# Kernel optimization log

Measured on AMD Instinct MI355X. Metric: run time of the kernel, lower is better.

Reference implementation:

```python
import jax, jax.numpy as jnp
import numpy as np

B, S, HID = 1, 4096, 2048
NH, NKV, D = 16, 4, 128           # num_heads, num_kv_heads, head_dim
QPG = NH // NKV                   # q heads per kv group
GROUP = (QPG + 2) * D             # fused per-group width: Q..Q K V
TOTAL = NKV * GROUP


def setup_inputs() -> dict:
    key = jax.random.key(0)
    k0, k1, k2 = jax.random.split(key, 3)
    x = jax.random.normal(k0, (B, S, HID), dtype=jnp.float32)
    weight_qkv = jax.random.normal(k1, (TOTAL, HID), dtype=jnp.float32) * 0.02
    weight_proj = jax.random.normal(k2, (HID, NH * D), dtype=jnp.float32) * 0.02
    return {"x": x, "weight_qkv": weight_qkv, "weight_proj": weight_proj}


def reference(x, weight_qkv, weight_proj):
    b, s, _ = x.shape
    # fused QKV projection, grouped layout: [b, s, NKV, (QPG+2)*D]
    qkv = jnp.einsum('bsh,ph->bsp', x, weight_qkv).reshape(b, s, NKV, GROUP)
    q = qkv[..., : QPG * D].reshape(b, s, NKV, QPG, D)      # [b,s,g,q,d]
    k = qkv[..., QPG * D:(QPG + 1) * D]                      # [b,s,g,d]
    v = qkv[..., (QPG + 1) * D:]                             # [b,s,g,d]

    scale = 1.0 / jnp.sqrt(jnp.float32(D))
    # GQA causal attention (ring attention at cp_size=1 == full causal attn)
    scores = jnp.einsum('bsgqd,btgd->bgqst', q, k) * scale   # [b,g,q,s,s]
    causal = jnp.tril(jnp.ones((s, s), dtype=bool))
    scores = jnp.where(causal, scores, jnp.finfo(scores.dtype).min)
    attn = jax.nn.softmax(scores, axis=-1)
    out = jnp.einsum('bgqst,btgd->bsgqd', attn, v)           # [b,s,g,q,d]
    out = out.reshape(b, s, NH * D)
    return jnp.einsum('bse,he->bsh', out, weight_proj)       # [b,s,HID]
```

## Files before the change

kernel.cpp:

```cpp
#include <hip/hip_runtime.h>
#include <hip/hip_bf16.h>
#include <stdint.h>

typedef __attribute__((ext_vector_type(8))) short short8;
typedef __attribute__((ext_vector_type(4))) float f32x4;

#define S_LEN   4096
#define HID_DIM 2048
#define NHEAD   16
#define NKV     4
#define DHEAD   128
#define QPG     4
#define GROUP   768
#define TOTAL   3072

#define NSLOT   336

__device__ __forceinline__ ushort f2bf(float f) {
    union { float f; uint32_t u; } c; c.f = f;
    uint32_t u = c.u;
    u += 0x7fff + ((u >> 16) & 1);
    return (ushort)(u >> 16);
}

__device__ __forceinline__ void gld_lds16(const void* g, void* l) {
    __builtin_amdgcn_global_load_lds(
        (const __attribute__((address_space(1))) void*)g,
        (__attribute__((address_space(3))) void*)l, 16, 0, 0);
}

__global__ __launch_bounds__(256)
void cvt_f32_bf16(const float* __restrict__ src, ushort* __restrict__ dst,
                  int n4, int mode)
{
    int i = blockIdx.x * blockDim.x + threadIdx.x;
    int stride = gridDim.x * blockDim.x;
    for (; i < n4; i += stride) {
        float sc = 1.0f;
        if (mode == 1) {
            int row = i >> 9;
            sc = ((row % GROUP) < QPG * DHEAD) ? 0.088388347648318447f : 1.0f;
        }
        float4 v = ((const float4*)src)[i];
        ushort4 o;
        o.x = f2bf(v.x * sc); o.y = f2bf(v.y * sc);
        o.z = f2bf(v.z * sc); o.w = f2bf(v.w * sc);
        ((ushort4*)dst)[i] = o;
    }
}

__global__ __launch_bounds__(256)
void zero_f4(float4* __restrict__ p, int n4)
{
    int i = blockIdx.x * blockDim.x + threadIdx.x;
    int stride = gridDim.x * blockDim.x;
    float4 z = {0.f, 0.f, 0.f, 0.f};
    for (; i < n4; i += stride) p[i] = z;
}

__device__ __forceinline__ void store_c(ushort* C, size_t idx, float v) { C[idx] = f2bf(v); }
__device__ __forceinline__ void store_c(float*  C, size_t idx, float v) { C[idx] = v; }

template <typename OutT, bool WRITE_VT>
__global__ __launch_bounds__(256, 2)
void gemm_bt(const ushort* __restrict__ A, const ushort* __restrict__ B,
             OutT* __restrict__ C, ushort* __restrict__ VT,
             int M, int N, int K)
{
    __shared__ alignas(16) ushort Asl[128 * 32];
    __shared__ alignas(16) ushort Bsl[128 * 32];

    const int tid  = threadIdx.x;
    const int wave = tid >> 6;
    const int lane = tid & 63;
    const int quad = lane >> 4;
    const int l15  = lane & 15;
    const int wr   = wave >> 1;
    const int wc   = wave & 1;
    const int m0   = blockIdx.y * 128;
    const int n0   = blockIdx.x * 128;

    f32x4 acc[4][4];
#pragma unroll
    for (int i = 0; i < 4; i++)
#pragma unroll
        for (int j = 0; j < 4; j++) acc[i][j] = (f32x4)0.0f;

    for (int kb = 0; kb < K; kb += 32) {
        __syncthreads();
#pragma unroll
        for (int r = 0; r < 2; r++) {
            int idx = tid + r * 256;
            int row = idx >> 2, c8 = idx & 3;
            char* la = (char*)Asl + (size_t)(wave * 64 + r * 256) * 16;
            char* lb = (char*)Bsl + (size_t)(wave * 64 + r * 256) * 16;
            gld_lds16(A + (size_t)(m0 + row) * K + kb + c8 * 8, la);
            gld_lds16(B + (size_t)(n0 + row) * K + kb + c8 * 8, lb);
        }
        __syncthreads();

        short8 af[4], bf[4];
#pragma unroll
        for (int i = 0; i < 4; i++)
            af[i] = *(const short8*)(&Asl[(wr * 64 + i * 16 + l15) * 32 + quad * 8]);
#pragma unroll
        for (int j = 0; j < 4; j++)
            bf[j] = *(const short8*)(&Bsl[(wc * 64 + j * 16 + l15) * 32 + quad * 8]);
#pragma unroll
        for (int i = 0; i < 4; i++)
#pragma unroll
            for (int j = 0; j < 4; j++)
                acc[i][j] = __builtin_amdgcn_mfma_f32_16x16x32_bf16(
                    af[i], bf[j], acc[i][j], 0, 0, 0);
    }

#pragma unroll
    for (int i = 0; i < 4; i++)
#pragma unroll
        for (int j = 0; j < 4; j++)
#pragma unroll
            for (int r = 0; r < 4; r++) {
                int row = m0 + wr * 64 + i * 16 + quad * 4 + r;
                int col = n0 + wc * 64 + j * 16 + l15;
                store_c(C, (size_t)row * N + col, acc[i][j][r]);
            }

    if (WRITE_VT) {
        int cb = n0 >> 7;
        if (cb % 6 == 5) {
            int g = cb / 6;
#pragma unroll
            for (int i = 0; i < 4; i++)
#pragma unroll
                for (int j = 0; j < 4; j++) {
                    int d    = wc * 64 + j * 16 + l15;
                    int row0 = m0 + wr * 64 + i * 16 + quad * 4;
                    ushort4 pk;
                    pk.x = f2bf(acc[i][j][0]); pk.y = f2bf(acc[i][j][1]);
                    pk.z = f2bf(acc[i][j][2]); pk.w = f2bf(acc[i][j][3]);
                    *(ushort4*)(VT + (size_t)(g * 128 + d) * S_LEN + row0) = pk;
                }
        }
    }
}

__global__ __launch_bounds__(256, 2)
void flash_attn(const ushort* __restrict__ qkv, const ushort* __restrict__ VT,
                ushort* __restrict__ out, float* __restrict__ o_slot,
                float* __restrict__ l_slot)
{
    const int b     = blockIdx.x;
    const int head  = b / 48;
    const int r48   = b - head * 48;
    const int pair  = r48 / 3;
    const int third = r48 - pair * 3;

    const int g    = head >> 2;
    const int qh   = head & 3;
    const int H    = 128 - 4 * pair;
    const int L    = 4 * pair + 4;
    const int c0   = third * 44;
    const int c1   = c0 + 44;

    const int tid  = threadIdx.x;
    const int wave = tid >> 6;
    const int lane = tid & 63;
    const int quad = lane >> 4;
    const int l15  = lane & 15;

    __shared__ alignas(16) ushort Kl[2][32][128];
    __shared__ alignas(16) ushort Vt[2][128][32];
    __shared__ alignas(16) ushort Pl[4][32][36];

    int seg_p[2], seg_t0[2], seg_t1[2], seg_slot[2];
    int nseg = 0;
    {
        int h1 = (c1 < H) ? c1 : H;
        if (c0 < h1) {
            seg_p[nseg] = 31 - pair; seg_t0[nseg] = c0; seg_t1[nseg] = h1;
            seg_slot[nseg] = head * 16 + pair;
            nseg++;
        }
        int l0 = (c0 > H) ? c0 : H;
        if (l0 < c1) {
            int lt0 = l0 - H, lt1 = c1 - H;
            int whole = (lt0 == 0) & (lt1 == L);
            seg_p[nseg] = pair; seg_t0[nseg] = lt0; seg_t1[nseg] = lt1;
            seg_slot[nseg] = whole ? -1 : (256 + head * 5 + (pair - 11));
            nseg++;
        }
    }

    const int koff = g * GROUP + QPG * DHEAD;

    for (int s = 0; s < nseg; s++) {
        const int t0 = seg_t0[s];
        const int t1 = seg_t1[s];
        const int q0 = seg_p[s] * 128;

        short8 qf[2][4];
#pragma unroll
        for (int mi = 0; mi < 2; mi++) {
            int row = q0 + wave * 32 + mi * 16 + l15;
            const ushort* qp = qkv + (size_t)row * TOTAL + g * GROUP + qh * DHEAD + quad * 8;
#pragma unroll
            for (int ks = 0; ks < 4; ks++)
                qf[mi][ks] = *(const short8*)(qp + ks * 32);
        }

        f32x4 o[2][8];
#pragma unroll
        for (int mi = 0; mi < 2; mi++)
#pragma unroll
            for (int df = 0; df < 8; df++) o[mi][df] = (f32x4)0.0f;
        float l_vec[2][4];
#pragma unroll
        for (int mi = 0; mi < 2; mi++)
#pragma unroll
            for (int r = 0; r < 4; r++) l_vec[mi][r] = 0.0f;

        const int kr = tid >> 4, kc = tid & 15;
        const int vd = tid >> 2, vc = tid & 3;

        float4 kpre[2], vpre[2];
#pragma unroll
        for (int r = 0; r < 2; r++) {
            kpre[r] = *(const float4*)(qkv + (size_t)(t0 * 32 + kr + r * 16) * TOTAL + koff + kc * 8);
            vpre[r] = *(const float4*)(VT + (size_t)(g * 128 + vd + r * 64) * S_LEN + t0 * 32 + vc * 8);
        }
#pragma unroll
        for (int r = 0; r < 2; r++) {
            int krow = kr + r * 16, vrow = vd + r * 64;
            *(float4*)(&Kl[0][krow][(kc ^ (krow & 7)) * 8]) = kpre[r];
            *(float4*)(&Vt[0][vrow][(vc ^ (vrow & 3)) * 8]) = vpre[r];
        }
        if (t0 + 1 < t1) {
            const int j1 = (t0 + 1) * 32;
#pragma unroll
            for (int r = 0; r < 2; r++) {
                kpre[r] = *(const float4*)(qkv + (size_t)(j1 + kr + r * 16) * TOTAL + koff + kc * 8);
                vpre[r] = *(const float4*)(VT + (size_t)(g * 128 + vd + r * 64) * S_LEN + j1 + vc * 8);
            }
        }
        __syncthreads();

        for (int t = t0; t < t1; t++) {
            const int cur = (t - t0) & 1;

            if (t + 1 < t1) {
#pragma unroll
                for (int r = 0; r < 2; r++) {
                    int krow = kr + r * 16, vrow = vd + r * 64;
                    *(float4*)(&Kl[cur ^ 1][krow][(kc ^ (krow & 7)) * 8]) = kpre[r];
                    *(float4*)(&Vt[cur ^ 1][vrow][(vc ^ (vrow & 3)) * 8]) = vpre[r];
                }
                if (t + 2 < t1) {
                    const int j2 = (t + 2) * 32;
#pragma unroll
                    for (int r = 0; r < 2; r++) {
                        kpre[r] = *(const float4*)(qkv + (size_t)(j2 + kr + r * 16) * TOTAL + koff + kc * 8);
                        vpre[r] = *(const float4*)(VT + (size_t)(g * 128 + vd + r * 64) * S_LEN + j2 + vc * 8);
                    }
                }
            }

            const int j0 = t * 32;
            f32x4 sacc[2][2];
#pragma unroll
            for (int mi = 0; mi < 2; mi++)
#pragma unroll
                for (int ni = 0; ni < 2; ni++) sacc[mi][ni] = (f32x4)0.0f;
            __builtin_amdgcn_s_setprio(1);
#pragma unroll
            for (int ni = 0; ni < 2; ni++)
#pragma unroll
                for (int ks = 0; ks < 4; ks++) {
                    int krow = ni * 16 + l15;
                    short8 kf = *(const short8*)(&Kl[cur][krow][((ks * 4 + quad) ^ (krow & 7)) * 8]);
#pragma unroll
                    for (int mi = 0; mi < 2; mi++)
                        sacc[mi][ni] = __builtin_amdgcn_mfma_f32_16x16x32_bf16(
                            qf[mi][ks], kf, sacc[mi][ni], 0, 0, 0);
                }
            __builtin_amdgcn_s_setprio(0);

#pragma unroll
            for (int mi = 0; mi < 2; mi++) {
                const int base = q0 + wave * 32 + mi * 16;
                if (j0 + 31 > base) {
#pragma unroll
                    for (int r = 0; r < 4; r++) {
                        int row_g = base + quad * 4 + r;
                        float rs = 0.0f;
#pragma unroll
                        for (int ni = 0; ni < 2; ni++) {
                            float e = __expf(sacc[mi][ni][r]);
                            int col_g = j0 + ni * 16 + l15;
                            e = (col_g > row_g) ? 0.0f : e;
                            sacc[mi][ni][r] = e;
                            rs += e;
                        }
                        l_vec[mi][r] += rs;
                    }
                } else {
#pragma unroll
                    for (int r = 0; r < 4; r++) {
                        float rs = 0.0f;
#pragma unroll
                        for (int ni = 0; ni < 2; ni++) {
                            float e = __expf(sacc[mi][ni][r]);
                            sacc[mi][ni][r] = e;
                            rs += e;
                        }
                        l_vec[mi][r] += rs;
                    }
                }
#pragma unroll
                for (int ni = 0; ni < 2; ni++)
#pragma unroll
                    for (int r = 0; r < 4; r++)
                        Pl[wave][mi * 16 + quad * 4 + r][ni * 16 + l15] =
                            f2bf(sacc[mi][ni][r]);
            }

            short8 pf[2];
#pragma unroll
            for (int mi = 0; mi < 2; mi++)
                pf[mi] = *(const short8*)(&Pl[wave][mi * 16 + l15][quad * 8]);
            __builtin_amdgcn_s_setprio(1);
#pragma unroll
            for (int df = 0; df < 8; df++) {
                int vrow = df * 16 + l15;
                short8 vf = *(const short8*)(&Vt[cur][vrow][(quad ^ (vrow & 3)) * 8]);
#pragma unroll
                for (int mi = 0; mi < 2; mi++)
                    o[mi][df] = __builtin_amdgcn_mfma_f32_16x16x32_bf16(
                        pf[mi], vf, o[mi][df], 0, 0, 0);
            }
            __builtin_amdgcn_s_setprio(0);

            __syncthreads();
        }

        if (seg_slot[s] >= 0) {
            const int sslot = seg_slot[s];
#pragma unroll
            for (int mi = 0; mi < 2; mi++)
#pragma unroll
                for (int r = 0; r < 4; r++) {
                    int row_l = wave * 32 + mi * 16 + quad * 4 + r;
                    float l = l_vec[mi][r];
                    l += __shfl_xor(l, 1);
                    l += __shfl_xor(l, 2);
                    l += __shfl_xor(l, 4);
                    l += __shfl_xor(l, 8);
                    if (l15 == 0)
                        atomicAdd(&l_slot[sslot * 128 + row_l], l);
#pragma unroll
                    for (int df = 0; df < 8; df++)
                        atomicAdd(&o_slot[((size_t)sslot * 128 + row_l) * 128
                                          + df * 16 + l15], o[mi][df][r]);
                }
        } else {
#pragma unroll
            for (int mi = 0; mi < 2; mi++)
#pragma unroll
                for (int r = 0; r < 4; r++) {
                    float l = l_vec[mi][r];
                    l += __shfl_xor(l, 1);
                    l += __shfl_xor(l, 2);
                    l += __shfl_xor(l, 4);
                    l += __shfl_xor(l, 8);
                    float inv = 1.0f / l;
                    int row = q0 + wave * 32 + mi * 16 + quad * 4 + r;
#pragma unroll
                    for (int df = 0; df < 8; df++) {
                        float v = o[mi][df][r] * inv;
                        out[(size_t)row * (NHEAD * DHEAD) + head * DHEAD
                            + df * 16 + l15] = f2bf(v);
                    }
                }
        }
    }
}

__global__ __launch_bounds__(256)
void fixup_norm(const float* __restrict__ o_slot, const float* __restrict__ l_slot,
                ushort* __restrict__ attn)
{
    const int slot = blockIdx.x;
    int head, q0;
    if (slot < 256) {
        head = slot >> 4;
        q0   = (31 - (slot & 15)) * 128;
    } else {
        int s = slot - 256;
        head = s / 5;
        q0   = (11 + (s - head * 5)) * 128;
    }
    const int t = threadIdx.x;
#pragma unroll 4
    for (int i = 0; i < 64; i++) {
        int idx = i * 256 + t;
        int row = idx >> 7, d = idx & 127;
        float l = l_slot[slot * 128 + row];
        float v = o_slot[(size_t)slot * 16384 + idx] / l;
        attn[(size_t)(q0 + row) * HID_DIM + head * DHEAD + d] = f2bf(v);
    }
}

extern "C" void kernel_launch(void* const* d_in, const int* in_sizes, int n_in,
                              void* d_out, int out_size, void* d_ws, size_t ws_size,
                              hipStream_t stream)
{
    const float* x     = (const float*)d_in[0];
    const float* wqkv  = (const float*)d_in[1];
    const float* wproj = (const float*)d_in[2];
    float* outp = (float*)d_out;

    const size_t n_x     = (size_t)S_LEN * HID_DIM;
    const size_t n_wqkv  = (size_t)TOTAL * HID_DIM;
    const size_t n_wproj = (size_t)HID_DIM * HID_DIM;
    const size_t n_qkv   = (size_t)S_LEN * TOTAL;
    const size_t n_attn  = (size_t)S_LEN * HID_DIM;

    ushort* xb     = (ushort*)d_ws;
    ushort* wqkvb  = xb + n_x;
    ushort* qkv    = wqkvb + n_wqkv;
    ushort* attn   = qkv + n_qkv;
    ushort* vt     = attn + n_attn;
    float* o_slot  = (float*)d_ws;
    float* l_slot  = o_slot + (size_t)NSLOT * 16384;
    ushort* wprojb = wqkvb;

    cvt_f32_bf16<<<2048, 256, 0, stream>>>(x, xb, (int)(n_x / 4), 0);
    cvt_f32_bf16<<<2048, 256, 0, stream>>>(wqkv, wqkvb, (int)(n_wqkv / 4), 1);

    gemm_bt<ushort, true><<<dim3(TOTAL / 128, S_LEN / 128), 256, 0, stream>>>(
        xb, wqkvb, qkv, vt, S_LEN, TOTAL, HID_DIM);

    zero_f4<<<2048, 256, 0, stream>>>((float4*)o_slot,
                                      (int)(((size_t)NSLOT * 16384 + NSLOT * 128) / 4));

    flash_attn<<<768, 256, 0, stream>>>(qkv, vt, attn, o_slot, l_slot);
    fixup_norm<<<NSLOT, 256, 0, stream>>>(o_slot, l_slot, attn);

    cvt_f32_bf16<<<2048, 256, 0, stream>>>(wproj, wprojb, (int)(n_wproj / 4), 0);
    gemm_bt<float, false><<<dim3(HID_DIM / 128, S_LEN / 128), 256, 0, stream>>>(
        attn, wprojb, outp, nullptr, S_LEN, HID_DIM, HID_DIM);
}
```

Before: 456.6 us.

## Compute transposed S^T tiles so P stays in registers, drop P LDS round-trip

The QK^T MFMA now has its operands swapped, so each lane holds a column of scores along the KV dimension. The exponentiated probabilities can then be packed straight into bf16 registers with v_cvt_pk_bf16 and fed to 16x16x16 MFMAs against V, with no round trip through the per-wave P scratch in LDS. The K and V tiles switch from XOR swizzling to padded rows. The end-of-iteration __syncthreads becomes an lgkmcnt wait plus s_barrier, and the output stores become 4-wide packed writes. The cost is twice as many smaller MFMAs for PV, and padded LDS rows that may leave some bank conflicts.

Measured after the change: 528.1 us. +15.7%, slower.

```diff
diff --git a/kernel.cpp b/kernel.cpp
--- a/kernel.cpp
+++ b/kernel.cpp
@@ -3,6 +3,7 @@
 #include <stdint.h>
 
 typedef __attribute__((ext_vector_type(8))) short short8;
+typedef __attribute__((ext_vector_type(4))) short bf16x4;
 typedef __attribute__((ext_vector_type(4))) float f32x4;
 
 #define S_LEN   4096
@@ -23,10 +24,20 @@
     return (ushort)(u >> 16);
 }
 
+__device__ __forceinline__ uint32_t cvt_pk_bf16(float lo, float hi) {
+    uint32_t r;
+    asm("v_cvt_pk_bf16_f32 %0, %1, %2" : "=v"(r) : "v"(lo), "v"(hi));
+    return r;
+}
+
 __device__ __forceinline__ void gld_lds16(const void* g, void* l) {
     __builtin_amdgcn_global_load_lds(
         (const __attribute__((address_space(1))) void*)g,
         (__attribute__((address_space(3))) void*)l, 16, 0, 0);
+}
+
+__device__ __forceinline__ void lds_barrier() {
+    asm volatile("s_waitcnt lgkmcnt(0)\n\ts_barrier" ::: "memory");
 }
 
 __global__ __launch_bounds__(256)
@@ -168,9 +179,8 @@
     const int quad = lane >> 4;
     const int l15  = lane & 15;
 
-    __shared__ alignas(16) ushort Kl[2][32][128];
-    __shared__ alignas(16) ushort Vt[2][128][32];
-    __shared__ alignas(16) ushort Pl[4][32][36];
+    __shared__ alignas(16) ushort Kl[2][32][136];
+    __shared__ alignas(16) ushort Vt[2][128][40];
 
     int seg_p[2], seg_t0[2], seg_t1[2], seg_slot[2];
     int nseg = 0;
@@ -200,24 +210,20 @@
 
         short8 qf[2][4];
 #pragma unroll
-        for (int mi = 0; mi < 2; mi++) {
-            int row = q0 + wave * 32 + mi * 16 + l15;
+        for (int qi = 0; qi < 2; qi++) {
+            int row = q0 + wave * 32 + qi * 16 + l15;
             const ushort* qp = qkv + (size_t)row * TOTAL + g * GROUP + qh * DHEAD + quad * 8;
 #pragma unroll
             for (int ks = 0; ks < 4; ks++)
-                qf[mi][ks] = *(const short8*)(qp + ks * 32);
+                qf[qi][ks] = *(const short8*)(qp + ks * 32);
         }
 
         f32x4 o[2][8];
 #pragma unroll
-        for (int mi = 0; mi < 2; mi++)
-#pragma unroll
-            for (int df = 0; df < 8; df++) o[mi][df] = (f32x4)0.0f;
-        float l_vec[2][4];
-#pragma unroll
-        for (int mi = 0; mi < 2; mi++)
-#pragma unroll
-            for (int r = 0; r < 4; r++) l_vec[mi][r] = 0.0f;
+        for (int qi = 0; qi < 2; qi++)
+#pragma unroll
+            for (int df = 0; df < 8; df++) o[qi][df] = (f32x4)0.0f;
+        float l_vec[2] = {0.0f, 0.0f};
 
         const int kr = tid >> 4, kc = tid & 15;
         const int vd = tid >> 2, vc = tid & 3;
@@ -230,9 +236,8 @@
         }
 #pragma unroll
         for (int r = 0; r < 2; r++) {
-            int krow = kr + r * 16, vrow = vd + r * 64;
-            *(float4*)(&Kl[0][krow][(kc ^ (krow & 7)) * 8]) = kpre[r];
-            *(float4*)(&Vt[0][vrow][(vc ^ (vrow & 3)) * 8]) = vpre[r];
+            *(float4*)(&Kl[0][kr + r * 16][kc * 8]) = kpre[r];
+            *(float4*)(&Vt[0][vd + r * 64][vc * 8]) = vpre[r];
         }
         if (t0 + 1 < t1) {
             const int j1 = (t0 + 1) * 32;
@@ -250,9 +255,8 @@
             if (t + 1 < t1) {
 #pragma unroll
                 for (int r = 0; r < 2; r++) {
-                    int krow = kr + r * 16, vrow = vd + r * 64;
-                    *(float4*)(&Kl[cur ^ 1][krow][(kc ^ (krow & 7)) * 8]) = kpre[r];
-                    *(float4*)(&Vt[cur ^ 1][vrow][(vc ^ (vrow & 3)) * 8]) = vpre[r];
+                    *(float4*)(&Kl[cur ^ 1][kr + r * 16][kc * 8]) = kpre[r];
+                    *(float4*)(&Vt[cur ^ 1][vd + r * 64][vc * 8]) = vpre[r];
                 }
                 if (t + 2 < t1) {
                     const int j2 = (t + 2) * 32;
@@ -267,119 +271,112 @@
             const int j0 = t * 32;
             f32x4 sacc[2][2];
 #pragma unroll
-            for (int mi = 0; mi < 2; mi++)
-#pragma unroll
-                for (int ni = 0; ni < 2; ni++) sacc[mi][ni] = (f32x4)0.0f;
+            for (int ki = 0; ki < 2; ki++)
+#pragma unroll
+                for (int qi = 0; qi < 2; qi++) sacc[ki][qi] = (f32x4)0.0f;
             __builtin_amdgcn_s_setprio(1);
 #pragma unroll
-            for (int ni = 0; ni < 2; ni++)
+            for (int ki = 0; ki < 2; ki++)
 #pragma unroll
                 for (int ks = 0; ks < 4; ks++) {
-                    int krow = ni * 16 + l15;
-                    short8 kf = *(const short8*)(&Kl[cur][krow][((ks * 4 + quad) ^ (krow & 7)) * 8]);
-#pragma unroll
-                    for (int mi = 0; mi < 2; mi++)
-                        sacc[mi][ni] = __builtin_amdgcn_mfma_f32_16x16x32_bf16(
-                            qf[mi][ks], kf, sacc[mi][ni], 0, 0, 0);
+                    short8 kf = *(const short8*)(&Kl[cur][ki * 16 + l15][ks * 32 + quad * 8]);
+#pragma unroll
+                    for (int qi = 0; qi < 2; qi++)
+                        sacc[ki][qi] = __builtin_amdgcn_mfma_f32_16x16x32_bf16(
+                            kf, qf[qi][ks], sacc[ki][qi], 0, 0, 0);
                 }
             __builtin_amdgcn_s_setprio(0);
 
-#pragma unroll
-            for (int mi = 0; mi < 2; mi++) {
-                const int base = q0 + wave * 32 + mi * 16;
-                if (j0 + 31 > base) {
-#pragma unroll
-                    for (int r = 0; r < 4; r++) {
-                        int row_g = base + quad * 4 + r;
-                        float rs = 0.0f;
-#pragma unroll
-                        for (int ni = 0; ni < 2; ni++) {
-                            float e = __expf(sacc[mi][ni][r]);
-                            int col_g = j0 + ni * 16 + l15;
-                            e = (col_g > row_g) ? 0.0f : e;
-                            sacc[mi][ni][r] = e;
+            bf16x4 pb[2][2];
+#pragma unroll
+            for (int qi = 0; qi < 2; qi++) {
+                const int qmin = q0 + wave * 32 + qi * 16;
+                float rs = 0.0f;
+                if (j0 + 31 > qmin) {
+                    const int q_g = qmin + l15;
+#pragma unroll
+                    for (int ki = 0; ki < 2; ki++)
+#pragma unroll
+                        for (int r = 0; r < 4; r++) {
+                            float e = __expf(sacc[ki][qi][r]);
+                            int kv_g = j0 + ki * 16 + quad * 4 + r;
+                            e = (kv_g > q_g) ? 0.0f : e;
+                            sacc[ki][qi][r] = e;
                             rs += e;
                         }
-                        l_vec[mi][r] += rs;
-                    }
                 } else {
 #pragma unroll
-                    for (int r = 0; r < 4; r++) {
-                        float rs = 0.0f;
-#pragma unroll
-                        for (int ni = 0; ni < 2; ni++) {
-                            float e = __expf(sacc[mi][ni][r]);
-                            sacc[mi][ni][r] = e;
+                    for (int ki = 0; ki < 2; ki++)
+#pragma unroll
+                        for (int r = 0; r < 4; r++) {
+                            float e = __expf(sacc[ki][qi][r]);
+                            sacc[ki][qi][r] = e;
                             rs += e;
                         }
-                        l_vec[mi][r] += rs;
-                    }
-                }
-#pragma unroll
-                for (int ni = 0; ni < 2; ni++)
-#pragma unroll
-                    for (int r = 0; r < 4; r++)
-                        Pl[wave][mi * 16 + quad * 4 + r][ni * 16 + l15] =
-                            f2bf(sacc[mi][ni][r]);
-            }
-
-            short8 pf[2];
-#pragma unroll
-            for (int mi = 0; mi < 2; mi++)
-                pf[mi] = *(const short8*)(&Pl[wave][mi * 16 + l15][quad * 8]);
+                }
+                l_vec[qi] += rs;
+#pragma unroll
+                for (int ki = 0; ki < 2; ki++) {
+                    union { uint32_t u[2]; bf16x4 v; } pw;
+                    pw.u[0] = cvt_pk_bf16(sacc[ki][qi][0], sacc[ki][qi][1]);
+                    pw.u[1] = cvt_pk_bf16(sacc[ki][qi][2], sacc[ki][qi][3]);
+                    pb[qi][ki] = pw.v;
+                }
+            }
+
             __builtin_amdgcn_s_setprio(1);
 #pragma unroll
             for (int df = 0; df < 8; df++) {
-                int vrow = df * 16 + l15;
-                short8 vf = *(const short8*)(&Vt[cur][vrow][(quad ^ (vrow & 3)) * 8]);
-#pragma unroll
-                for (int mi = 0; mi < 2; mi++)
-                    o[mi][df] = __builtin_amdgcn_mfma_f32_16x16x32_bf16(
-                        pf[mi], vf, o[mi][df], 0, 0, 0);
+#pragma unroll
+                for (int ki = 0; ki < 2; ki++) {
+                    bf16x4 vf = *(const bf16x4*)(&Vt[cur][df * 16 + l15][ki * 16 + quad * 4]);
+#pragma unroll
+                    for (int qi = 0; qi < 2; qi++)
+                        asm("v_mfma_f32_16x16x16_bf16 %0, %1, %2, %0"
+                            : "+v"(o[qi][df]) : "v"(vf), "v"(pb[qi][ki]));
+                }
             }
             __builtin_amdgcn_s_setprio(0);
 
-            __syncthreads();
+            lds_barrier();
         }
 
         if (seg_slot[s] >= 0) {
             const int sslot = seg_slot[s];
 #pragma unroll
-            for (int mi = 0; mi < 2; mi++)
-#pragma unroll
-                for (int r = 0; r < 4; r++) {
-                    int row_l = wave * 32 + mi * 16 + quad * 4 + r;
-                    float l = l_vec[mi][r];
-                    l += __shfl_xor(l, 1);
-                    l += __shfl_xor(l, 2);
-                    l += __shfl_xor(l, 4);
-                    l += __shfl_xor(l, 8);
-                    if (l15 == 0)
-                        atomicAdd(&l_slot[sslot * 128 + row_l], l);
-#pragma unroll
-                    for (int df = 0; df < 8; df++)
+            for (int qi = 0; qi < 2; qi++) {
+                float l = l_vec[qi];
+                l += __shfl_xor(l, 16);
+                l += __shfl_xor(l, 32);
+                int row_l = wave * 32 + qi * 16 + l15;
+                if (lane < 16)
+                    atomicAdd(&l_slot[sslot * 128 + row_l], l);
+#pragma unroll
+                for (int df = 0; df < 8; df++)
+#pragma unroll
+                    for (int r = 0; r < 4; r++)
                         atomicAdd(&o_slot[((size_t)sslot * 128 + row_l) * 128
-                                          + df * 16 + l15], o[mi][df][r]);
-                }
+                                          + df * 16 + quad * 4 + r], o[qi][df][r]);
+            }
         } else {
 #pragma unroll
-            for (int mi = 0; mi < 2; mi++)
-#pragma unroll
-                for (int r = 0; r < 4; r++) {
-                    float l = l_vec[mi][r];
-                    l += __shfl_xor(l, 1);
-                    l += __shfl_xor(l, 2);
-                    l += __shfl_xor(l, 4);
-                    l += __shfl_xor(l, 8);
-                    float inv = 1.0f / l;
-                    int row = q0 + wave * 32 + mi * 16 + quad * 4 + r;
-#pragma unroll
-                    for (int df = 0; df < 8; df++) {
-                        float v = o[mi][df][r] * inv;
-                        out[(size_t)row * (NHEAD * DHEAD) + head * DHEAD
-                            + df * 16 + l15] = f2bf(v);
-                    }
-                }
+            for (int qi = 0; qi < 2; qi++) {
+                float l = l_vec[qi];
+                l += __shfl_xor(l, 16);
+                l += __shfl_xor(l, 32);
+                float inv = 1.0f / l;
+                int row = q0 + wave * 32 + qi * 16 + l15;
+#pragma unroll
+                for (int df = 0; df < 8; df++) {
+                    ushort4 pk4;
+                    pk4.x = f2bf(o[qi][df][0] * inv);
+                    pk4.y = f2bf(o[qi][df][1] * inv);
+                    pk4.z = f2bf(o[qi][df][2] * inv);
+                    pk4.w = f2bf(o[qi][df][3] * inv);
+                    *(ushort4*)(out + (size_t)row * (NHEAD * DHEAD) + head * DHEAD
+                                + df * 16 + quad * 4) = pk4;
+                }
+            }
         }
     }
 }
```
